# Kernel tuning notes

Hardware: AMD Instinct MI355X
Metric: run time of the kernel (lower is better)

Reference implementation:

```python
import jax, jax.numpy as jnp
import numpy as np

B, SQ, SD, H = 64, 64, 512, 128


def setup_inputs() -> dict:
    key = jax.random.key(0)
    k1, k2, k3, k4, k5 = jax.random.split(key, 5)
    q = jax.random.normal(k1, (B, SQ, H), dtype=jnp.float32)
    d_pos = jax.random.normal(k2, (B, SD, H), dtype=jnp.float32)
    d_neg = jax.random.normal(k3, (B, SD, H), dtype=jnp.float32)
    mask_pos = jax.random.randint(k4, (B, SD), 0, 2, dtype=jnp.int32).at[:, 0].set(1)
    mask_neg = jax.random.randint(k5, (B, SD), 0, 2, dtype=jnp.int32).at[:, 0].set(1)
    return {"q": q, "d_pos": d_pos, "d_neg": d_neg,
            "mask_pos": mask_pos, "mask_neg": mask_neg}


def _colbert_maxsim(q, d, mask):
    # q: [a, s, h], d: [b, t, h], mask: [b, t] -> scores [a, b]
    simis = jnp.einsum('ash,bth->abst', q, d)            # [a, b, s, t]
    simis = jnp.where(mask[None, :, None, :] == 0, -jnp.inf, simis)
    return simis.max(axis=3).sum(axis=2)                 # max over t, sum over s


def reference(q, d_pos, d_neg, mask_pos, mask_neg):
    # Concatenate pos and in-batch-negative score blocks -> [B, 2B]
    distances = jnp.concatenate(
        [_colbert_maxsim(q, d_pos, mask_pos),
         _colbert_maxsim(q, d_neg, mask_neg)], axis=1)
    labels = jnp.arange(q.shape[0])
    logp = jax.nn.log_softmax(distances, axis=1)
    loss = -jnp.take_along_axis(logp, labels[:, None], axis=1).mean()
    return loss
```

## Files before the change

### kernel.cpp

```cpp
#include <hip/hip_runtime.h>
#include <hip/hip_bf16.h>
#include <math.h>
#include <stdint.h>

#define BB 64
#define SQN 64
#define SDN 512
#define HH 128

typedef __attribute__((ext_vector_type(8))) short bf16x8;
typedef __attribute__((ext_vector_type(16))) float f32x16;

__device__ __forceinline__ short f2bf(float f) {
  union { float f; unsigned u; } x; x.f = f;
  unsigned r = x.u + 0x7fffu + ((x.u >> 16) & 1u);
  return (short)(r >> 16);
}

__device__ __forceinline__ void gl_lds16(const short* g, short* l) {
  __builtin_amdgcn_global_load_lds(
      (const __attribute__((address_space(1))) unsigned int*)g,
      (__attribute__((address_space(3))) unsigned int*)l, 16, 0, 0);
}

__global__ __launch_bounds__(64)
void compact_meta(const int* __restrict__ mp, const int* __restrict__ mn,
                  int* __restrict__ perm, int* __restrict__ nchunks,
                  int* __restrict__ nvalid) {
  const int b = blockIdx.x, side = blockIdx.y;
  const int* mask = side ? mn : mp;
  const int ln = threadIdx.x;
  const int base = (side * BB + b) * SDN;
  int run = 0;
  #pragma unroll
  for (int it = 0; it < SDN / 64; ++it) {
    int t = it * 64 + ln;
    int m = mask[b * SDN + t];
    unsigned long long bal = __ballot(m != 0);
    int pos = run + __popcll(bal & ((1ull << ln) - 1ull));
    if (m) perm[base + pos] = t;
    run += (int)__popcll(bal);
  }
  int pad = (run + 127) & ~127;
  for (int j = run + ln; j < pad; j += 64) perm[base + j] = -1;
  if (ln == 0) {
    nchunks[side * BB + b] = pad >> 7;
    nvalid[side * BB + b]  = run;
  }
}

__global__ __launch_bounds__(256)
void convert_all(const float* __restrict__ q, const float* __restrict__ dp,
                 const float* __restrict__ dn, const int* __restrict__ perm,
                 const int* __restrict__ nchunks,
                 short* __restrict__ oq, short* __restrict__ od) {
  const int D_BLOCKS = (2 * BB * SDN) / 8;
  if (blockIdx.x < D_BLOCKS) {
    int gid = blockIdx.x * 8 + (threadIdx.x >> 5);
    int l32 = threadIdx.x & 31;
    int bs = gid >> 9;
    int j  = gid & 511;
    if (j >= (nchunks[bs] << 7)) return;
    int side = bs >> 6, b = bs & 63;
    int src_t = perm[bs * SDN + j];
    const float* srcmat = side ? dn : dp;
    float4 v = make_float4(0.f, 0.f, 0.f, 0.f);
    if (src_t >= 0)
      v = ((const float4*)(srcmat + ((size_t)b * SDN + src_t) * HH))[l32];
    short4 o; o.x = f2bf(v.x); o.y = f2bf(v.y); o.z = f2bf(v.z); o.w = f2bf(v.w);
    *(short4*)&od[((size_t)bs * SDN + j) * HH + l32 * 4] = o;
  } else {
    int i = (blockIdx.x - D_BLOCKS) * 256 + threadIdx.x;
    float4 v = ((const float4*)q)[i];
    short4 o; o.x = f2bf(v.x); o.y = f2bf(v.y); o.z = f2bf(v.z); o.w = f2bf(v.w);
    *(short4*)&oq[i * 4] = o;
  }
}

__global__ __launch_bounds__(256, 2)
void maxsim_kernel(const short* __restrict__ qb,
                   const short* __restrict__ dc,
                   const int* __restrict__ nchunks,
                   const int* __restrict__ nvalid,
                   float* __restrict__ scores) {
  const int lid  = blockIdx.x + 16 * blockIdx.y;
  const int xcd  = lid & 7;
  const int slot = lid >> 3;
  const int aslc = slot & 15;
  const int bs0  = (xcd + 8 * (slot >> 4)) * 4;

  __shared__ __align__(16) short d_lds[2][128 * 128];

  const int tid = threadIdx.x;
  const int ln  = tid & 63;
  const int w   = tid >> 6;
  const int l31 = ln & 31;
  const int kh  = ln >> 5;
  const int a   = aslc * 4 + w;

  int nchv[4], nvv[4];
  #pragma unroll
  for (int i = 0; i < 4; ++i) {
    nchv[i] = nchunks[bs0 + i];
    nvv[i]  = nvalid[bs0 + i];
  }

  bf16x8 qfrag[2][8];
  #pragma unroll
  for (int half = 0; half < 2; ++half) {
    const short* qrow = qb + ((size_t)a * SQN + half * 32 + l31) * HH + kh * 8;
    #pragma unroll
    for (int kc = 0; kc < 8; ++kc)
      qfrag[half][kc] = *(const bf16x8*)(qrow + kc * 16);
  }

  float rmaxh[2] = {0.f, 0.f};

  {
    const short* dsrc = dc + (size_t)bs0 * SDN * HH;
    #pragma unroll
    for (int it = 0; it < 8; ++it) {
      int f = it * 256 + tid;
      int row = f >> 4;
      int c = (f & 15) ^ (row & 15);
      gl_lds16(&dsrc[row * HH + c * 8], &d_lds[0][(it * 256 + w * 64) * 8]);
    }
  }
  __syncthreads();

  int bi = 0, tc = 0, buf = 0;
  for (;;) {
    int nbi = bi, ntc = tc + 1;
    if (ntc == nchv[bi]) { ntc = 0; nbi = bi + 1; }
    const bool hn = (nbi < 4);

    if (hn) {
      const short* dsrc = dc + ((size_t)(bs0 + nbi) * SDN + ntc * 128) * HH;
      short* dst = &d_lds[buf ^ 1][0];
      #pragma unroll
      for (int it = 0; it < 8; ++it) {
        int f = it * 256 + tid;
        int row = f >> 4;
        int c = (f & 15) ^ (row & 15);
        gl_lds16(&dsrc[row * HH + c * 8], &dst[(it * 256 + w * 64) * 8]);
      }
    }

    const int ntt = (tc == nchv[bi] - 1)
                        ? ((nvv[bi] - (tc << 7) + 31) >> 5)
                        : 4;
    const short* bufp = &d_lds[buf][0];
    #pragma unroll
    for (int tt = 0; tt < 4; ++tt) {
      if (tt < ntt) {
        int trow = tt * 32 + l31;
        int tm = trow & 15;
        const short* bbase = &bufp[trow * HH];
        f32x16 acc0 = {0,0,0,0,0,0,0,0,0,0,0,0,0,0,0,0};
        f32x16 acc1 = {0,0,0,0,0,0,0,0,0,0,0,0,0,0,0,0};
        #pragma unroll
        for (int kc = 0; kc < 8; ++kc) {
          int c = (kc * 2 + kh) ^ tm;
          bf16x8 dfrag = *(const bf16x8*)&bbase[c * 8];
          acc0 = __builtin_amdgcn_mfma_f32_32x32x16_bf16(dfrag, qfrag[0][kc], acc0, 0, 0, 0);
          acc1 = __builtin_amdgcn_mfma_f32_32x32x16_bf16(dfrag, qfrag[1][kc], acc1, 0, 0, 0);
        }
        float m0 = acc0[0], m1 = acc1[0];
        #pragma unroll
        for (int r = 1; r < 16; ++r) {
          m0 = fmaxf(m0, acc0[r]);
          m1 = fmaxf(m1, acc1[r]);
        }
        rmaxh[0] = fmaxf(rmaxh[0], m0);
        rmaxh[1] = fmaxf(rmaxh[1], m1);
      }
    }

    if (ntc == 0) {
      float v0 = fmaxf(rmaxh[0], __shfl_xor(rmaxh[0], 32));
      float v1 = fmaxf(rmaxh[1], __shfl_xor(rmaxh[1], 32));
      float s = v0 + v1;
      s += __shfl_xor(s, 1);  s += __shfl_xor(s, 2);  s += __shfl_xor(s, 4);
      s += __shfl_xor(s, 8);  s += __shfl_xor(s, 16);
      if (ln == 0) scores[(size_t)a * (2 * BB) + bs0 + bi] = s;
      rmaxh[0] = 0.f; rmaxh[1] = 0.f;
    }

    __syncthreads();
    if (!hn) break;
    bi = nbi; tc = ntc; buf ^= 1;
  }
}

__global__ __launch_bounds__(1024)
void loss_kernel(const float* __restrict__ scores, float* __restrict__ out) {
  __shared__ float part[16];
  const int tid = threadIdx.x;
  const int ln = tid & 63;
  const int w  = tid >> 6;
  float acc = 0.f;
  #pragma unroll
  for (int i = 0; i < 4; ++i) {
    int r = w * 4 + i;
    float v0 = scores[r * 128 + ln];
    float v1 = scores[r * 128 + 64 + ln];
    float mx = fmaxf(v0, v1);
    #pragma unroll
    for (int off = 32; off >= 1; off >>= 1) mx = fmaxf(mx, __shfl_xor(mx, off));
    float e = __expf(v0 - mx) + __expf(v1 - mx);
    #pragma unroll
    for (int off = 32; off >= 1; off >>= 1) e += __shfl_xor(e, off);
    float lse = mx + __logf(e);
    float diag = __shfl(v0, r);
    acc += lse - diag;
  }
  if (ln == 0) part[w] = acc;
  __syncthreads();
  if (w == 0) {
    float v = (ln < 16) ? part[ln] : 0.f;
    #pragma unroll
    for (int off = 8; off >= 1; off >>= 1) v += __shfl_xor(v, off);
    if (ln == 0) out[0] = v * (1.0f / 64.0f);
  }
}

extern "C" void kernel_launch(void* const* d_in, const int* in_sizes, int n_in,
                              void* d_out, int out_size, void* d_ws, size_t ws_size,
                              hipStream_t stream) {
  const float* q        = (const float*)d_in[0];
  const float* d_pos    = (const float*)d_in[1];
  const float* d_neg    = (const float*)d_in[2];
  const int*   mask_pos = (const int*)d_in[3];
  const int*   mask_neg = (const int*)d_in[4];

  short* q_bf = (short*)d_ws;
  short* d_c  = q_bf + (size_t)BB * SQN * HH;
  int*   perm = (int*)(d_c + (size_t)2 * BB * SDN * HH);
  int*   nchunks = perm + 2 * BB * SDN;
  int*   nvalid  = nchunks + 128;
  float* scores  = (float*)(nvalid + 128);

  compact_meta<<<dim3(BB, 2), 64, 0, stream>>>(mask_pos, mask_neg, perm,
                                               nchunks, nvalid);

  const int D_BLOCKS = (2 * BB * SDN) / 8;
  const int Q_BLOCKS = (BB * SQN * HH / 4) / 256;
  convert_all<<<D_BLOCKS + Q_BLOCKS, 256, 0, stream>>>(q, d_pos, d_neg, perm,
                                                       nchunks, q_bf, d_c);

  dim3 grid(16 , 32 );
  maxsim_kernel<<<grid, 256, 0, stream>>>(q_bf, d_c, nchunks, nvalid, scores);

  loss_kernel<<<1, 1024, 0, stream>>>(scores, (float*)d_out);
}
```

Before: 126.5 us.

## Fuse mask compaction into convert and loss into maxsim via last-block ticket

Removes the separate compaction kernel by having each convert block recompute the mask prefix scan for its own 8 rows. The loss computation moves into maxsim_kernel and is run by whichever block takes the last ticket from a global atomic counter. Padding is reduced to 32-row granularity, so d loads for partial chunks skip unused rows. This drops two kernel launches and the perm round-trip through global memory. The cost is redundant mask scans in every convert block and a serial loss tail on one block.

```diff
diff --git a/kernel.cpp b/kernel.cpp
--- a/kernel.cpp
+++ b/kernel.cpp
@@ -23,46 +23,54 @@
       (__attribute__((address_space(3))) unsigned int*)l, 16, 0, 0);
 }
 
-__global__ __launch_bounds__(64)
-void compact_meta(const int* __restrict__ mp, const int* __restrict__ mn,
-                  int* __restrict__ perm, int* __restrict__ nchunks,
-                  int* __restrict__ nvalid) {
-  const int b = blockIdx.x, side = blockIdx.y;
-  const int* mask = side ? mn : mp;
-  const int ln = threadIdx.x;
-  const int base = (side * BB + b) * SDN;
-  int run = 0;
-  #pragma unroll
-  for (int it = 0; it < SDN / 64; ++it) {
-    int t = it * 64 + ln;
-    int m = mask[b * SDN + t];
-    unsigned long long bal = __ballot(m != 0);
-    int pos = run + __popcll(bal & ((1ull << ln) - 1ull));
-    if (m) perm[base + pos] = t;
-    run += (int)__popcll(bal);
-  }
-  int pad = (run + 127) & ~127;
-  for (int j = run + ln; j < pad; j += 64) perm[base + j] = -1;
-  if (ln == 0) {
-    nchunks[side * BB + b] = pad >> 7;
-    nvalid[side * BB + b]  = run;
-  }
-}
-
 __global__ __launch_bounds__(256)
 void convert_all(const float* __restrict__ q, const float* __restrict__ dp,
-                 const float* __restrict__ dn, const int* __restrict__ perm,
-                 const int* __restrict__ nchunks,
-                 short* __restrict__ oq, short* __restrict__ od) {
+                 const float* __restrict__ dn,
+                 const int* __restrict__ mp, const int* __restrict__ mn,
+                 short* __restrict__ oq, short* __restrict__ od,
+                 int* __restrict__ nchunks, int* __restrict__ nvalid,
+                 int* __restrict__ counter) {
   const int D_BLOCKS = (2 * BB * SDN) / 8;
   if (blockIdx.x < D_BLOCKS) {
-    int gid = blockIdx.x * 8 + (threadIdx.x >> 5);
-    int l32 = threadIdx.x & 31;
-    int bs = gid >> 9;
-    int j  = gid & 511;
-    if (j >= (nchunks[bs] << 7)) return;
-    int side = bs >> 6, b = bs & 63;
-    int src_t = perm[bs * SDN + j];
+    const int bs = blockIdx.x >> 6;
+    const int j0 = (blockIdx.x & 63) * 8;
+    const int side = bs >> 6, b = bs & 63;
+    const int* mask = (side ? mn : mp) + b * SDN;
+
+    __shared__ int s_perm[8];
+    __shared__ int s_pad32;
+
+    if (threadIdx.x < 64) {
+      const int ln = threadIdx.x;
+      int mreg[8];
+      #pragma unroll
+      for (int it = 0; it < 8; ++it) mreg[it] = mask[it * 64 + ln];
+      int run = 0;
+      #pragma unroll
+      for (int it = 0; it < 8; ++it) {
+        unsigned long long bal = __ballot(mreg[it] != 0);
+        int pos = run + __popcll(bal & ((1ull << ln) - 1ull));
+        if (mreg[it]) {
+          unsigned rel = (unsigned)(pos - j0);
+          if (rel < 8u) s_perm[rel] = it * 64 + ln;
+        }
+        run += (int)__popcll(bal);
+      }
+      if (ln < 8 && j0 + ln >= run) s_perm[ln] = -1;
+      if (ln == 0) {
+        s_pad32 = (run + 31) & ~31;
+        if (j0 == 0) {
+          nchunks[bs] = ((run + 127) & ~127) >> 7;
+          nvalid[bs]  = run;
+        }
+      }
+    }
+    __syncthreads();
+
+    const int j = j0 + (threadIdx.x >> 5);
+    if (j >= s_pad32) return;
+    const int l32 = threadIdx.x & 31;
+    const int src_t = s_perm[threadIdx.x >> 5];
     const float* srcmat = side ? dn : dp;
     float4 v = make_float4(0.f, 0.f, 0.f, 0.f);
     if (src_t >= 0)
@@ -70,19 +78,25 @@
     short4 o; o.x = f2bf(v.x); o.y = f2bf(v.y); o.z = f2bf(v.z); o.w = f2bf(v.w);
     *(short4*)&od[((size_t)bs * SDN + j) * HH + l32 * 4] = o;
   } else {
+    if (blockIdx.x == D_BLOCKS && threadIdx.x == 0) *counter = 0;
     int i = (blockIdx.x - D_BLOCKS) * 256 + threadIdx.x;
     float4 v = ((const float4*)q)[i];
     short4 o; o.x = f2bf(v.x); o.y = f2bf(v.y); o.z = f2bf(v.z); o.w = f2bf(v.w);
     *(short4*)&oq[i * 4] = o;
   }
 }
+
+#define ITS_OF(bi_, tc_) \
+  (((tc_) == nchv[bi_] - 1) ? (((nvv[bi_] - ((tc_) << 7) + 31) >> 5) << 1) : 8)
 
 __global__ __launch_bounds__(256, 2)
 void maxsim_kernel(const short* __restrict__ qb,
                    const short* __restrict__ dc,
                    const int* __restrict__ nchunks,
                    const int* __restrict__ nvalid,
-                   float* __restrict__ scores) {
+                   float* __restrict__ scores,
+                   int* __restrict__ counter,
+                   float* __restrict__ out) {
   const int lid  = blockIdx.x + 16 * blockIdx.y;
   const int xcd  = lid & 7;
   const int slot = lid >> 3;
@@ -116,14 +130,18 @@
 
   float rmaxh[2] = {0.f, 0.f};
 
+  int cur_its = ITS_OF(0, 0);
+
   {
     const short* dsrc = dc + (size_t)bs0 * SDN * HH;
     #pragma unroll
     for (int it = 0; it < 8; ++it) {
-      int f = it * 256 + tid;
-      int row = f >> 4;
-      int c = (f & 15) ^ (row & 15);
-      gl_lds16(&dsrc[row * HH + c * 8], &d_lds[0][(it * 256 + w * 64) * 8]);
+      if (it < cur_its) {
+        int f = it * 256 + tid;
+        int row = f >> 4;
+        int c = (f & 15) ^ (row & 15);
+        gl_lds16(&dsrc[row * HH + c * 8], &d_lds[0][(it * 256 + w * 64) * 8]);
+      }
     }
   }
   __syncthreads();
@@ -133,22 +151,23 @@
     int nbi = bi, ntc = tc + 1;
     if (ntc == nchv[bi]) { ntc = 0; nbi = bi + 1; }
     const bool hn = (nbi < 4);
+    const int nxt_its = hn ? ITS_OF(nbi, ntc) : 0;
 
     if (hn) {
       const short* dsrc = dc + ((size_t)(bs0 + nbi) * SDN + ntc * 128) * HH;
       short* dst = &d_lds[buf ^ 1][0];
       #pragma unroll
       for (int it = 0; it < 8; ++it) {
-        int f = it * 256 + tid;
-        int row = f >> 4;
-        int c = (f & 15) ^ (row & 15);
-        gl_lds16(&dsrc[row * HH + c * 8], &dst[(it * 256 + w * 64) * 8]);
-      }
-    }
-
-    const int ntt = (tc == nchv[bi] - 1)
-                        ? ((nvv[bi] - (tc << 7) + 31) >> 5)
-                        : 4;
+        if (it < nxt_its) {
+          int f = it * 256 + tid;
+          int row = f >> 4;
+          int c = (f & 15) ^ (row & 15);
+          gl_lds16(&dsrc[row * HH + c * 8], &dst[(it * 256 + w * 64) * 8]);
+        }
+      }
+    }
+
+    const int ntt = cur_its >> 1;
     const short* bufp = &d_lds[buf][0];
     #pragma unroll
     for (int tt = 0; tt < 4; ++tt) {
@@ -188,33 +207,40 @@
 
     __syncthreads();
     if (!hn) break;
-    bi = nbi; tc = ntc; buf ^= 1;
-  }
-}
-
-__global__ __launch_bounds__(1024)
-void loss_kernel(const float* __restrict__ scores, float* __restrict__ out) {
+    bi = nbi; tc = ntc; buf ^= 1; cur_its = nxt_its;
+  }
+
+  __threadfence();
+  __shared__ int s_ticket;
+  if (tid == 0) s_ticket = atomicAdd(counter, 1);
+  __syncthreads();
+  if (s_ticket != 511) return;
+  __threadfence();
+
   __shared__ float part[16];
-  const int tid = threadIdx.x;
-  const int ln = tid & 63;
-  const int w  = tid >> 6;
-  float acc = 0.f;
   #pragma unroll
-  for (int i = 0; i < 4; ++i) {
-    int r = w * 4 + i;
-    float v0 = scores[r * 128 + ln];
-    float v1 = scores[r * 128 + 64 + ln];
-    float mx = fmaxf(v0, v1);
-    #pragma unroll
-    for (int off = 32; off >= 1; off >>= 1) mx = fmaxf(mx, __shfl_xor(mx, off));
-    float e = __expf(v0 - mx) + __expf(v1 - mx);
-    #pragma unroll
-    for (int off = 32; off >= 1; off >>= 1) e += __shfl_xor(e, off);
-    float lse = mx + __logf(e);
-    float diag = __shfl(v0, r);
-    acc += lse - diag;
-  }
-  if (ln == 0) part[w] = acc;
+  for (int q8 = 0; q8 < 4; ++q8) {
+    int vp = w * 4 + q8;
+    float acc = 0.f;
+    #pragma unroll
+    for (int i = 0; i < 4; ++i) {
+      int r = vp * 4 + i;
+      float v0 = __hip_atomic_load(&scores[r * 128 + ln],
+                                   __ATOMIC_RELAXED, __HIP_MEMORY_SCOPE_AGENT);
+      float v1 = __hip_atomic_load(&scores[r * 128 + 64 + ln],
+                                   __ATOMIC_RELAXED, __HIP_MEMORY_SCOPE_AGENT);
+      float mx = fmaxf(v0, v1);
+      #pragma unroll
+      for (int off = 32; off >= 1; off >>= 1) mx = fmaxf(mx, __shfl_xor(mx, off));
+      float e = __expf(v0 - mx) + __expf(v1 - mx);
+      #pragma unroll
+      for (int off = 32; off >= 1; off >>= 1) e += __shfl_xor(e, off);
+      float lse = mx + __logf(e);
+      float diag = __shfl(v0, r);
+      acc += lse - diag;
+    }
+    if (ln == 0) part[vp] = acc;
+  }
   __syncthreads();
   if (w == 0) {
     float v = (ln < 16) ? part[ln] : 0.f;
@@ -235,21 +261,17 @@
 
   short* q_bf = (short*)d_ws;
   short* d_c  = q_bf + (size_t)BB * SQN * HH;
-  int*   perm = (int*)(d_c + (size_t)2 * BB * SDN * HH);
-  int*   nchunks = perm + 2 * BB * SDN;
+  int*   nchunks = (int*)(d_c + (size_t)2 * BB * SDN * HH);
   int*   nvalid  = nchunks + 128;
   float* scores  = (float*)(nvalid + 128);
-
-  compact_meta<<<dim3(BB, 2), 64, 0, stream>>>(mask_pos, mask_neg, perm,
-                                               nchunks, nvalid);
+  int*   counter = (int*)(scores + 64 * 128);
 
   const int D_BLOCKS = (2 * BB * SDN) / 8;
   const int Q_BLOCKS = (BB * SQN * HH / 4) / 256;
-  convert_all<<<D_BLOCKS + Q_BLOCKS, 256, 0, stream>>>(q, d_pos, d_neg, perm,
-                                                       nchunks, q_bf, d_c);
+  convert_all<<<D_BLOCKS + Q_BLOCKS, 256, 0, stream>>>(
+      q, d_pos, d_neg, mask_pos, mask_neg, q_bf, d_c, nchunks, nvalid, counter);
 
   dim3 grid(16 , 32 );
-  maxsim_kernel<<<grid, 256, 0, stream>>>(q_bf, d_c, nchunks, nvalid, scores);
-
-  loss_kernel<<<1, 1024, 0, stream>>>(scores, (float*)d_out);
-}
+  maxsim_kernel<<<grid, 256, 0, stream>>>(q_bf, d_c, nchunks, nvalid, scores,
+                                          counter, (float*)d_out);
+}
```

After: 155.5 us. +22.9%, slower.
